# Performance work log

Measured on AMD Instinct MI355X. Metric: run time of the kernel, lower is better.

Reference implementation:

```python
import jax, jax.numpy as jnp
import numpy as np

N, E = 50000, 800000
IN_CH, HID, OUT = 128, 64, 64
H1, H2 = 4, 1
NEG_SLOPE = 0.2  # PyG GATConv default


def _glorot(key, shape):
    fan_in, fan_out = shape[0], shape[-1]
    lim = (6.0 / (fan_in + fan_out)) ** 0.5
    return jax.random.uniform(key, shape, jnp.float32, -lim, lim)


def setup_inputs() -> dict:
    key = jax.random.key(0)
    ks = jax.random.split(key, 12)
    x = jax.random.normal(ks[0], (N, IN_CH), jnp.float32)
    edge_index = jax.random.randint(ks[1], (2, E), 0, N, jnp.int64)
    # layer 1: in_ch -> hid, 4 heads, concat
    W1 = _glorot(ks[2], (IN_CH, H1 * HID))
    a_src1 = _glorot(ks[3], (H1, HID))
    a_dst1 = _glorot(ks[4], (H1, HID))
    b1 = jnp.zeros((H1 * HID,), jnp.float32)
    # layer 2: hid*4 -> out, 1 head, mean (concat=False)
    W2 = _glorot(ks[5], (H1 * HID, H2 * OUT))
    a_src2 = _glorot(ks[6], (H2, OUT))
    a_dst2 = _glorot(ks[7], (H2, OUT))
    b2 = jnp.zeros((OUT,), jnp.float32)
    return {"x": x, "edge_index": edge_index, "W1": W1, "a_src1": a_src1,
            "a_dst1": a_dst1, "b1": b1, "W2": W2, "a_src2": a_src2,
            "a_dst2": a_dst2, "b2": b2}


def gat_layer(x, src, dst, W, a_src, a_dst, b, concat):
    n = x.shape[0]
    Hh, Fh = a_src.shape
    h = (x @ W).reshape(n, Hh, Fh)                      # [N,H,F]
    al_src = jnp.sum(h * a_src[None], axis=-1)          # [N,H]
    al_dst = jnp.sum(h * a_dst[None], axis=-1)          # [N,H]
    logits = jax.nn.leaky_relu(al_src[src] + al_dst[dst], NEG_SLOPE)  # [E,H]
    # numerically stable segment softmax over destination nodes
    mx = jax.ops.segment_max(logits, dst, num_segments=n)
    mx = jnp.where(jnp.isfinite(mx), mx, 0.0)
    e = jnp.exp(logits - mx[dst])                       # [E,H]
    denom = jax.ops.segment_sum(e, dst, num_segments=n)  # [N,H]
    alpha = e / jnp.maximum(denom[dst], 1e-16)          # [E,H]
    msg = h[src] * alpha[:, :, None]                    # [E,H,F]
    out = jax.ops.segment_sum(msg, dst, num_segments=n)  # [N,H,F]
    out = out.reshape(n, Hh * Fh) if concat else out.mean(axis=1)
    return out + b


def reference(x, edge_index, W1, a_src1, a_dst1, b1, W2, a_src2, a_dst2, b2):
    n = x.shape[0]
    # PyG GATConv adds self-loops by default
    loops = jnp.arange(n, dtype=edge_index.dtype)
    src = jnp.concatenate([edge_index[0], loops])
    dst = jnp.concatenate([edge_index[1], loops])
    h = gat_layer(x, src, dst, W1, a_src1, a_dst1, b1, concat=True)
    h = jax.nn.elu(h)
    # dropout is identity in eval mode
    out = gat_layer(h, src, dst, W2, a_src2, a_dst2, b2, concat=False)
    return out
```

## Files before the change

kernel.cpp:

```cpp
#include <hip/hip_runtime.h>
#include <math.h>

#define NEG_SLOPE 0.2f
#define SLOTS 64
#define PARTB 256

typedef unsigned short ushort_t;
typedef _Float16 f16x8 __attribute__((ext_vector_type(8)));
typedef _Float16 h2v  __attribute__((ext_vector_type(2)));
typedef float f32x4v __attribute__((ext_vector_type(4)));

__device__ __forceinline__ float leaky(float x) { return x > 0.f ? x : NEG_SLOPE * x; }

__device__ __forceinline__ ushort_t f2h(float f) {
    union { _Float16 h; ushort_t u; } v; v.h = (_Float16)f; return v.u;
}
__device__ __forceinline__ unsigned packh(float a, float b) {
    union { h2v h; unsigned u; } c; c.h[0] = (_Float16)a; c.h[1] = (_Float16)b; return c.u;
}

__global__ __launch_bounds__(256) void k_prep0A(const float* __restrict__ W1, const float* __restrict__ W2,
                                                const float* __restrict__ as1, const float* __restrict__ ad1,
                                                const float* __restrict__ as2, const float* __restrict__ ad2,
                                                ushort_t* __restrict__ W1t, ushort_t* __restrict__ W2t,
                                                float* __restrict__ va1s, float* __restrict__ va1d,
                                                float* __restrict__ va2s, float* __restrict__ va2d,
                                                const int* __restrict__ ei, int E, int CH, int NBKT,
                                                int* __restrict__ bcnt) {
    __shared__ int hist[256];
    int b = blockIdx.x, t = threadIdx.x;
    if (b >= 322) {
        int k = b - 322;
        hist[t] = 0;
        __syncthreads();
        int i0 = k * CH;
        for (int it = 0; it < CH; it += 256) {
            int i = i0 + it + t;
            if (it + t < CH && i < E) atomicAdd(&hist[ei[E + i] >> 8], 1);
        }
        __syncthreads();
        if (t < NBKT) bcnt[t * PARTB + k] = hist[t];
        return;
    }
    if (b < 256) {
        if (t < 128) W1t[b * 128 + t] = f2h(W1[t * 256 + b]);
    } else if (b < 320) {
        int n = b - 256;
        W2t[n * 256 + t] = f2h(W2[t * 64 + n]);
    } else if (b == 320) {
        for (int idx = t; idx < 1024; idx += 256) {
            int k = idx >> 3, h = (idx >> 1) & 3, sd = idx & 1;
            const float* a = sd ? ad1 : as1;
            float acc = 0.f;
            for (int f = 0; f < 64; ++f) acc += W1[k * 256 + h * 64 + f] * a[h * 64 + f];
            (sd ? va1d : va1s)[k * 4 + h] = acc;
        }
    } else {
        for (int idx = t; idx < 512; idx += 256) {
            int k = idx >> 1, sd = idx & 1;
            const float* a = sd ? ad2 : as2;
            float acc = 0.f;
            for (int f = 0; f < 64; ++f) acc += W2[k * 64 + f] * a[f];
            (sd ? va2d : va2s)[k] = acc;
        }
    }
}

__global__ __launch_bounds__(256) void k_partB1(const int* __restrict__ bcnt,
                                                int* __restrict__ offs, int* __restrict__ btot) {
    __shared__ int wsum[4];
    int t = threadIdx.x, b = blockIdx.x;
    int c = bcnt[b * PARTB + t];
    int lane = t & 63, w = t >> 6;
    int v = c;
    #pragma unroll
    for (int off = 1; off < 64; off <<= 1) {
        int u = __shfl_up(v, off, 64);
        if (lane >= off) v += u;
    }
    if (lane == 63) wsum[w] = v;
    __syncthreads();
    int add = 0;
    for (int ww = 0; ww < w; ++ww) add += wsum[ww];
    offs[b * PARTB + t] = v - c + add;
    if (t == 255) btot[b] = v + add;
}

__global__ __launch_bounds__(256) void k_partB2(const int* __restrict__ btot,
                                                int* __restrict__ bstart, int NBKT, int E) {
    __shared__ int wsum[4];
    int t = threadIdx.x;
    int c = (t < NBKT) ? btot[t] : 0;
    int lane = t & 63, w = t >> 6;
    int v = c;
    #pragma unroll
    for (int off = 1; off < 64; off <<= 1) {
        int u = __shfl_up(v, off, 64);
        if (lane >= off) v += u;
    }
    if (lane == 63) wsum[w] = v;
    __syncthreads();
    int add = 0;
    for (int ww = 0; ww < w; ++ww) add += wsum[ww];
    if (t < NBKT) bstart[t] = v - c + add;
    if (t == 0) bstart[NBKT] = E;
}

__global__ __launch_bounds__(256) void k_partCx(const int* __restrict__ ei, int E, int CH, int NBKT,
                                                const int* __restrict__ offs, const int* __restrict__ bstart,
                                                unsigned* __restrict__ epk,
                                                const float* __restrict__ x,
                                                const float* __restrict__ va1s, const float* __restrict__ va1d,
                                                ushort_t* __restrict__ xh,
                                                float4* __restrict__ alS, float4* __restrict__ alD, int N) {
    __shared__ int cur[256];
    int b = blockIdx.x, t = threadIdx.x;
    if (b < PARTB) {
        int k = b;
        if (t < NBKT) cur[t] = bstart[t] + offs[t * PARTB + k];
        __syncthreads();
        int i0 = k * CH;
        for (int it = 0; it < CH; it += 256) {
            int i = i0 + it + t;
            if (it + t < CH && i < E) {
                unsigned s = (unsigned)ei[i];
                unsigned d = (unsigned)ei[E + i];
                int pos = atomicAdd(&cur[d >> 8], 1);
                epk[pos] = (d << 16) | s;
            }
        }
        return;
    }
    int bb = b - PARTB;
    int r = bb * 16 + (t >> 4);
    int idx = t & 15;
    if (r >= N) return;
    const float* xr = x + (size_t)r * 128 + idx * 8;
    float4 f0 = *(const float4*)xr;
    float4 f1 = *(const float4*)(xr + 4);
    uint4 pv;
    pv.x = packh(f0.x, f0.y); pv.y = packh(f0.z, f0.w);
    pv.z = packh(f1.x, f1.y); pv.w = packh(f1.z, f1.w);
    *(uint4*)&xh[(size_t)r * 128 + idx * 8] = pv;
    float xs[8] = {f0.x, f0.y, f0.z, f0.w, f1.x, f1.y, f1.z, f1.w};
    float s0 = 0, s1 = 0, s2 = 0, s3 = 0, d0 = 0, d1 = 0, d2 = 0, d3 = 0;
    #pragma unroll
    for (int j = 0; j < 8; ++j) {
        int k = idx * 8 + j;
        float4 vs = *(const float4*)&va1s[k * 4];
        float4 vd = *(const float4*)&va1d[k * 4];
        s0 += xs[j] * vs.x; s1 += xs[j] * vs.y; s2 += xs[j] * vs.z; s3 += xs[j] * vs.w;
        d0 += xs[j] * vd.x; d1 += xs[j] * vd.y; d2 += xs[j] * vd.z; d3 += xs[j] * vd.w;
    }
    #pragma unroll
    for (int off = 8; off >= 1; off >>= 1) {
        s0 += __shfl_xor(s0, off, 64); s1 += __shfl_xor(s1, off, 64);
        s2 += __shfl_xor(s2, off, 64); s3 += __shfl_xor(s3, off, 64);
        d0 += __shfl_xor(d0, off, 64); d1 += __shfl_xor(d1, off, 64);
        d2 += __shfl_xor(d2, off, 64); d3 += __shfl_xor(d3, off, 64);
    }
    if (idx == 0) {
        alS[r] = make_float4(s0, s1, s2, s3);
        alD[r] = make_float4(d0, d1, d2, d3);
    }
}

__global__ __launch_bounds__(256) void k_partD(const unsigned* __restrict__ epk, const int* __restrict__ bstart,
                                               int* __restrict__ cnt, ushort_t* __restrict__ csr, int N) {
    __shared__ ushort_t rows[256 * SLOTS];
    __shared__ int cl[256];
    int b = blockIdx.x, t = threadIdx.x;
    for (int i = t; i < 256 * SLOTS / 8; i += 256)
        *(uint4*)&rows[(size_t)i * 8] = make_uint4(0, 0, 0, 0);
    cl[t] = 0;
    __syncthreads();
    int n0 = b * 256;
    if (n0 + t < N) rows[t * SLOTS] = (ushort_t)(n0 + t);
    int e0 = bstart[b], e1 = bstart[b + 1];
    for (int i = e0 + t; i < e1; i += 256) {
        unsigned u = epk[i];
        int dl = (u >> 16) & 255;
        int slot = atomicAdd(&cl[dl], 1);
        if (slot < SLOTS - 1) rows[dl * SLOTS + 1 + slot] = (ushort_t)(u & 0xFFFFu);
    }
    __syncthreads();
    int nvalid = N - n0; if (nvalid > 256) nvalid = 256;
    size_t gbase = (size_t)n0 * SLOTS;
    for (int i = t; i < nvalid * SLOTS / 8; i += 256)
        *(uint4*)(csr + gbase + (size_t)i * 8) = *(const uint4*)&rows[(size_t)i * 8];
    if (t < nvalid) {
        int c = cl[t]; if (c > SLOTS - 1) c = SLOTS - 1;
        cnt[n0 + t] = c;
    }
}

#define CONS(p, a) do { \
    _Float16 ah_ = (_Float16)(a); \
    h2v a2_ = {ah_, ah_}; \
    union { uint4 u; h2v h[4]; } c_; c_.u = (p); \
    ha0 += c_.h[0] * a2_; ha1 += c_.h[1] * a2_; \
    ha2 += c_.h[2] * a2_; ha3 += c_.h[3] * a2_; } while (0)

#define FLUSH() do { \
    acc[0] += (float)ha0[0]; acc[1] += (float)ha0[1]; \
    acc[2] += (float)ha1[0]; acc[3] += (float)ha1[1]; \
    acc[4] += (float)ha2[0]; acc[5] += (float)ha2[1]; \
    acc[6] += (float)ha3[0]; acc[7] += (float)ha3[1]; \
    ha0 = (h2v)0; ha1 = (h2v)0; ha2 = (h2v)0; ha3 = (h2v)0; } while (0)

__global__ __launch_bounds__(256) void k_agg1(const int* __restrict__ cnt, const ushort_t* __restrict__ csr,
                                              const float4* __restrict__ alS4, const float4* __restrict__ alD4,
                                              const ushort_t* __restrict__ xh,
                                              ushort_t* __restrict__ aggh, int N) {
    __shared__ float s_alpha[4][SLOTS][4];
    __shared__ int   s_off[4][SLOTS];
    int w = threadIdx.x >> 6, lane = threadIdx.x & 63;
    int n = blockIdx.x * 4 + w;
    if (n >= N) return;
    int stored = cnt[n]; if (stored > SLOTS - 1) stored = SLOTS - 1;
    int deg = stored + 1;
    int s = 0;
    if (lane < deg) s = csr[(size_t)n * SLOTS + lane];
    s_off[w][lane] = (lane < deg) ? (s << 8) : 0;

    float e0 = 0.f, e1 = 0.f, e2 = 0.f, e3 = 0.f;
    if (lane < deg) {
        float4 ald = alD4[n];
        float4 as = alS4[s];
        e0 = __expf(leaky(as.x + ald.x));
        e1 = __expf(leaky(as.y + ald.y));
        e2 = __expf(leaky(as.z + ald.z));
        e3 = __expf(leaky(as.w + ald.w));
    }
    *(float4*)&s_alpha[w][lane][0] = make_float4(e0, e1, e2, e3);

    int head = lane >> 4, cid = lane & 15;
    const char* xb = (const char*)xh + cid * 16;

    float acc[8];
    #pragma unroll
    for (int i = 0; i < 8; ++i) acc[i] = 0.f;
    h2v ha0 = (h2v)0, ha1 = (h2v)0, ha2 = (h2v)0, ha3 = (h2v)0;

    int nit = (deg + 3) & ~3;

    int4 ovA = *(const int4*)&s_off[w][0];
    uint4 pA0 = *(const uint4*)(xb + ovA.x);
    uint4 pA1 = *(const uint4*)(xb + ovA.y);
    uint4 pA2 = *(const uint4*)(xb + ovA.z);
    uint4 pA3 = *(const uint4*)(xb + ovA.w);

    for (int j = 0; j < nit; j += 8) {
        uint4 pB0, pB1, pB2, pB3;
        bool hasB = (j + 4 < nit);
        if (hasB) {
            int4 ovB = *(const int4*)&s_off[w][j + 4];
            pB0 = *(const uint4*)(xb + ovB.x);
            pB1 = *(const uint4*)(xb + ovB.y);
            pB2 = *(const uint4*)(xb + ovB.z);
            pB3 = *(const uint4*)(xb + ovB.w);
        }
        {
            float a0 = s_alpha[w][j + 0][head];
            float a1 = s_alpha[w][j + 1][head];
            float a2 = s_alpha[w][j + 2][head];
            float a3 = s_alpha[w][j + 3][head];
            CONS(pA0, a0); CONS(pA1, a1); CONS(pA2, a2); CONS(pA3, a3);
        }
        if (hasB) {
            if (j + 8 < nit) {
                int4 ovA2 = *(const int4*)&s_off[w][j + 8];
                pA0 = *(const uint4*)(xb + ovA2.x);
                pA1 = *(const uint4*)(xb + ovA2.y);
                pA2 = *(const uint4*)(xb + ovA2.z);
                pA3 = *(const uint4*)(xb + ovA2.w);
            }
            float a0 = s_alpha[w][j + 4][head];
            float a1 = s_alpha[w][j + 5][head];
            float a2 = s_alpha[w][j + 6][head];
            float a3 = s_alpha[w][j + 7][head];
            CONS(pB0, a0); CONS(pB1, a1); CONS(pB2, a2); CONS(pB3, a3);
        }
        FLUSH();
    }

    float d0 = e0, d1 = e1, d2 = e2, d3 = e3;
    #pragma unroll
    for (int off = 32; off >= 1; off >>= 1) {
        d0 += __shfl_xor(d0, off, 64); d1 += __shfl_xor(d1, off, 64);
        d2 += __shfl_xor(d2, off, 64); d3 += __shfl_xor(d3, off, 64);
    }
    float dh = head == 0 ? d0 : head == 1 ? d1 : head == 2 ? d2 : d3;
    float inv = 1.f / fmaxf(dh, 1e-16f);

    uint4 u;
    u.x = packh(acc[0] * inv, acc[1] * inv);
    u.y = packh(acc[2] * inv, acc[3] * inv);
    u.z = packh(acc[4] * inv, acc[5] * inv);
    u.w = packh(acc[6] * inv, acc[7] * inv);
    *(uint4*)(aggh + (size_t)n * 512 + head * 128 + cid * 8) = u;
}
#undef CONS
#undef FLUSH

__global__ __launch_bounds__(256) void k_g1(const ushort_t* __restrict__ aggh, const ushort_t* __restrict__ W1t,
                                            const float* __restrict__ b1,
                                            const float* __restrict__ va2s, const float* __restrict__ va2d,
                                            ushort_t* __restrict__ out1h,
                                            float* __restrict__ al2S, float* __restrict__ al2D, int N) {
    __shared__ ushort_t sU[4 * 32 * 136];
    __shared__ float s_al2w[4][32][2];
    int t = threadIdx.x;
    int w = t >> 6, lane = t & 63;
    int m = lane & 15, quad = lane >> 4;
    int r0 = blockIdx.x * 32;

    #pragma unroll
    for (int q = 0; q < 8; ++q) {
        int idx = t + q * 256;
        int row = idx >> 6, off = idx & 63;
        int gr = r0 + row;
        uint4 v = (gr < N) ? *(const uint4*)(aggh + (size_t)gr * 512 + off * 8)
                           : make_uint4(0, 0, 0, 0);
        int h = off >> 4, k8 = off & 15;
        *(uint4*)&sU[(size_t)(h * 32 + row) * 136 + k8 * 8] = v;
    }
    __syncthreads();

    f32x4v acc[2][4];
    #pragma unroll
    for (int r = 0; r < 2; ++r)
        #pragma unroll
        for (int cg = 0; cg < 4; ++cg) acc[r][cg] = (f32x4v){0.f, 0.f, 0.f, 0.f};
    #pragma unroll
    for (int ks = 0; ks < 4; ++ks) {
        f16x8 af[2];
        #pragma unroll
        for (int r = 0; r < 2; ++r)
            af[r] = *(f16x8*)&sU[(size_t)(w * 32 + r * 16 + m) * 136 + ks * 32 + quad * 8];
        #pragma unroll
        for (int cg = 0; cg < 4; ++cg) {
            f16x8 bf = *(f16x8*)&W1t[(size_t)(w * 64 + cg * 16 + m) * 128 + ks * 32 + quad * 8];
            #pragma unroll
            for (int r = 0; r < 2; ++r)
                acc[r][cg] = __builtin_amdgcn_mfma_f32_16x16x32_f16(af[r], bf, acc[r][cg], 0, 0, 0);
        }
    }

    float ps[2][4], pd[2][4];
    #pragma unroll
    for (int r = 0; r < 2; ++r)
        #pragma unroll
        for (int reg = 0; reg < 4; ++reg) { ps[r][reg] = 0.f; pd[r][reg] = 0.f; }
    #pragma unroll
    for (int cg = 0; cg < 4; ++cg) {
        int c = w * 64 + cg * 16 + m;
        float bias = b1[c];
        float v2s = va2s[c], v2d = va2d[c];
        #pragma unroll
        for (int r = 0; r < 2; ++r)
            #pragma unroll
            for (int reg = 0; reg < 4; ++reg) {
                int row = r * 16 + quad * 4 + reg;
                int gr = r0 + row;
                float v = acc[r][cg][reg] + bias;
                v = v > 0.f ? v : (__expf(v) - 1.f);
                if (gr < N) out1h[(size_t)gr * 256 + c] = f2h(v);
                ps[r][reg] += v * v2s;
                pd[r][reg] += v * v2d;
            }
    }
    #pragma unroll
    for (int off = 1; off <= 8; off <<= 1)
        #pragma unroll
        for (int r = 0; r < 2; ++r)
            #pragma unroll
            for (int reg = 0; reg < 4; ++reg) {
                ps[r][reg] += __shfl_xor(ps[r][reg], off, 64);
                pd[r][reg] += __shfl_xor(pd[r][reg], off, 64);
            }
    if (m == 0) {
        #pragma unroll
        for (int r = 0; r < 2; ++r)
            #pragma unroll
            for (int reg = 0; reg < 4; ++reg) {
                int row = r * 16 + quad * 4 + reg;
                s_al2w[w][row][0] = ps[r][reg];
                s_al2w[w][row][1] = pd[r][reg];
            }
    }
    __syncthreads();
    if (t < 32) {
        int gr = r0 + t;
        if (gr < N) {
            float a = 0.f, b = 0.f;
            #pragma unroll
            for (int w2 = 0; w2 < 4; ++w2) { a += s_al2w[w2][t][0]; b += s_al2w[w2][t][1]; }
            al2S[gr] = a; al2D[gr] = b;
        }
    }
}

__global__ __launch_bounds__(256) void k_g2(const ushort_t* __restrict__ in, const ushort_t* __restrict__ W2t,
                                            ushort_t* __restrict__ h2h, int N) {
    __shared__ ushort_t As[64 * 136];
    __shared__ ushort_t Bs[64 * 136];
    int t = threadIdx.x;
    int r0 = blockIdx.x * 64;
    int w = t >> 6, lane = t & 63;
    int m = lane & 15, quad = lane >> 4;
    f32x4v acc[4];
    #pragma unroll
    for (int r = 0; r < 4; ++r) acc[r] = (f32x4v){0.f, 0.f, 0.f, 0.f};
    for (int kb = 0; kb < 2; ++kb) {
        #pragma unroll
        for (int q = 0; q < 4; ++q) {
            int idx = t + q * 256;
            int row = idx >> 4, off = idx & 15;
            int gr = r0 + row;
            uint4 v = (gr < N) ? *(const uint4*)(in + (size_t)gr * 256 + kb * 128 + off * 8)
                               : make_uint4(0, 0, 0, 0);
            *(uint4*)&As[row * 136 + off * 8] = v;
        }
        #pragma unroll
        for (int q = 0; q < 4; ++q) {
            int idx = t + q * 256;
            int row = idx >> 4, off = idx & 15;
            uint4 v = *(const uint4*)(W2t + (size_t)row * 256 + kb * 128 + off * 8);
            *(uint4*)&Bs[row * 136 + off * 8] = v;
        }
        __syncthreads();
        #pragma unroll
        for (int ks = 0; ks < 4; ++ks) {
            int k0 = ks * 32 + quad * 8;
            f16x8 af[4], bfr;
            #pragma unroll
            for (int r = 0; r < 4; ++r) af[r] = *(f16x8*)&As[(r * 16 + m) * 136 + k0];
            bfr = *(f16x8*)&Bs[(w * 16 + m) * 136 + k0];
            #pragma unroll
            for (int r = 0; r < 4; ++r)
                acc[r] = __builtin_amdgcn_mfma_f32_16x16x32_f16(af[r], bfr, acc[r], 0, 0, 0);
        }
        __syncthreads();
    }
    int col = w * 16 + m;
    #pragma unroll
    for (int r = 0; r < 4; ++r) {
        int gr0 = r0 + r * 16 + quad * 4;
        #pragma unroll
        for (int reg = 0; reg < 4; ++reg) {
            int gr = gr0 + reg;
            if (gr < N) h2h[(size_t)gr * 64 + col] = f2h(acc[r][reg]);
        }
    }
}

__global__ __launch_bounds__(256) void k_agg2(const int* __restrict__ cnt, const ushort_t* __restrict__ csr,
                                              const float* __restrict__ alS, const float* __restrict__ alD,
                                              const ushort_t* __restrict__ h2h, const float* __restrict__ b2,
                                              float* __restrict__ out, int N) {
    int lane = threadIdx.x & 63;
    int n = blockIdx.x * 4 + (threadIdx.x >> 6);
    if (n >= N) return;
    int stored = cnt[n]; if (stored > SLOTS - 1) stored = SLOTS - 1;
    int deg = stored + 1;
    const ushort_t* crow = csr + (size_t)n * SLOTS;

    int s0 = 0;
    if (lane < deg) s0 = crow[lane];

    int grp = lane >> 3, cid = lane & 7;
    int choff = cid * 16;
    const char* hbase = (const char*)h2h;

    uint4 pbuf[3];
    #pragma unroll
    for (int i = 0; i < 3; ++i) {
        int sj = __shfl(s0, i * 8 + grp, 64);
        pbuf[i] = *(const uint4*)(hbase + ((size_t)sj << 7) + choff);
    }

    float ald = alD[n];
    float e0 = 0.f;
    if (lane < deg) e0 = __expf(leaky(alS[s0] + ald));

    h2v ha0 = (h2v)0, ha1 = (h2v)0, ha2 = (h2v)0, ha3 = (h2v)0;
    #pragma unroll
    for (int i = 0; i < 3; ++i) {
        float a = __shfl(e0, i * 8 + grp, 64);
        union { uint4 u; h2v h[4]; } c; c.u = pbuf[i];
        _Float16 ah = (_Float16)a;
        h2v a2 = {ah, ah};
        ha0 += c.h[0] * a2; ha1 += c.h[1] * a2;
        ha2 += c.h[2] * a2; ha3 += c.h[3] * a2;
    }
    for (int j = 24; j < deg; j += 8) {
        int jj = j + grp;
        float a = __shfl(e0, jj, 64);
        int sj = __shfl(s0, jj, 64);
        union { uint4 u; h2v h[4]; } c;
        c.u = *(const uint4*)(hbase + ((size_t)sj << 7) + choff);
        _Float16 ah = (_Float16)a;
        h2v a2 = {ah, ah};
        ha0 += c.h[0] * a2; ha1 += c.h[1] * a2;
        ha2 += c.h[2] * a2; ha3 += c.h[3] * a2;
    }

    float den = e0;
    #pragma unroll
    for (int off = 32; off >= 1; off >>= 1) den += __shfl_xor(den, off, 64);
    float inv = 1.f / fmaxf(den, 1e-16f);

    float acc[8];
    acc[0] = (float)ha0[0]; acc[1] = (float)ha0[1];
    acc[2] = (float)ha1[0]; acc[3] = (float)ha1[1];
    acc[4] = (float)ha2[0]; acc[5] = (float)ha2[1];
    acc[6] = (float)ha3[0]; acc[7] = (float)ha3[1];
    #pragma unroll
    for (int off = 8; off <= 32; off <<= 1)
        #pragma unroll
        for (int i = 0; i < 8; ++i) acc[i] += __shfl_xor(acc[i], off, 64);

    if (grp == 0) {
        int c8 = cid * 8;
        float4 b0 = *(const float4*)&b2[c8];
        float4 b1v = *(const float4*)&b2[c8 + 4];
        float4 o0 = make_float4(acc[0]*inv + b0.x, acc[1]*inv + b0.y, acc[2]*inv + b0.z, acc[3]*inv + b0.w);
        float4 o1 = make_float4(acc[4]*inv + b1v.x, acc[5]*inv + b1v.y, acc[6]*inv + b1v.z, acc[7]*inv + b1v.w);
        *(float4*)(out + (size_t)n * 64 + c8) = o0;
        *(float4*)(out + (size_t)n * 64 + c8 + 4) = o1;
    }
}

extern "C" void kernel_launch(void* const* d_in, const int* in_sizes, int n_in,
                              void* d_out, int out_size, void* d_ws, size_t ws_size,
                              hipStream_t stream) {
    const float* x      = (const float*)d_in[0];
    const int*   ei     = (const int*)d_in[1];
    const float* W1     = (const float*)d_in[2];
    const float* a_src1 = (const float*)d_in[3];
    const float* a_dst1 = (const float*)d_in[4];
    const float* b1     = (const float*)d_in[5];
    const float* W2     = (const float*)d_in[6];
    const float* a_src2 = (const float*)d_in[7];
    const float* a_dst2 = (const float*)d_in[8];
    const float* b2     = (const float*)d_in[9];
    float* out = (float*)d_out;

    int N = in_sizes[0] / 128;
    int E = in_sizes[1] / 2;

    char* ws = (char*)d_ws;
    size_t off = 0;
    auto alloc = [&](size_t bytes) -> void* {
        void* p = ws + off;
        off = (off + bytes + 255) & ~(size_t)255;
        return p;
    };
    ushort_t* xh    = (ushort_t*)alloc((size_t)N * 128 * 2);
    ushort_t* aggh  = (ushort_t*)alloc((size_t)N * 512 * 2);
    ushort_t* out1h = (ushort_t*)alloc((size_t)N * 256 * 2);
    ushort_t* h2h   = (ushort_t*)alloc((size_t)N * 64 * 2);
    ushort_t* W1t   = (ushort_t*)alloc(256 * 128 * 2);
    ushort_t* W2t   = (ushort_t*)alloc(64 * 256 * 2);
    float* va1s  = (float*)alloc(128 * 4 * 4);
    float* va1d  = (float*)alloc(128 * 4 * 4);
    float* va2s  = (float*)alloc(256 * 4);
    float* va2d  = (float*)alloc(256 * 4);
    float* alS1  = (float*)alloc((size_t)N * 4 * 4);
    float* alD1  = (float*)alloc((size_t)N * 4 * 4);
    float* alS2  = (float*)alloc((size_t)N * 4);
    float* alD2  = (float*)alloc((size_t)N * 4);
    int*   cnt   = (int*)alloc((size_t)N * 4);
    ushort_t* csr = (ushort_t*)alloc((size_t)N * SLOTS * 2);
    int NBKT = (N + 255) >> 8;
    int*      bcnt  = (int*)alloc((size_t)NBKT * PARTB * 4);
    int*      offs  = (int*)alloc((size_t)NBKT * PARTB * 4);
    int*      btot  = (int*)alloc((size_t)NBKT * 4);
    int*      bstart= (int*)alloc((size_t)(NBKT + 1) * 4);
    unsigned* epk   = (unsigned*)alloc((size_t)E * 4);
    (void)ws_size; (void)n_in; (void)out_size;

    int CH  = (E + PARTB - 1) / PARTB;
    int XB  = (N + 15) / 16;
    int AB1 = (N + 3) / 4;
    int G1  = (N + 31) / 32;
    int G2  = (N + 63) / 64;
    int NC4 = (N + 3) / 4;

    k_prep0A<<<322 + PARTB, 256, 0, stream>>>(W1, W2, a_src1, a_dst1, a_src2, a_dst2,
                                              W1t, W2t, va1s, va1d, va2s, va2d,
                                              ei, E, CH, NBKT, bcnt);
    k_partB1<<<NBKT, 256, 0, stream>>>(bcnt, offs, btot);
    k_partB2<<<1, 256, 0, stream>>>(btot, bstart, NBKT, E);
    k_partCx<<<PARTB + XB, 256, 0, stream>>>(ei, E, CH, NBKT, offs, bstart, epk,
                                             x, va1s, va1d, xh, (float4*)alS1, (float4*)alD1, N);
    k_partD<<<NBKT, 256, 0, stream>>>(epk, bstart, cnt, csr, N);
    k_agg1<<<AB1, 256, 0, stream>>>(cnt, csr,
                                    (const float4*)alS1, (const float4*)alD1,
                                    xh, aggh, N);
    k_g1<<<G1, 256, 0, stream>>>(aggh, W1t, b1, va2s, va2d, out1h, alS2, alD2, N);
    k_g2<<<G2, 256, 0, stream>>>(out1h, W2t, h2h, N);
    k_agg2<<<NC4, 256, 0, stream>>>(cnt, csr, alS2, alD2, h2h, b2, out, N);
}
```

Before: 238.6 us.

## Fuse graph-build prep kernels into one persistent kernel with grid barriers

Merges the five preprocessing kernels (histogram/transpose, two scans, scatter plus x conversion, CSR build) into one 256-block kernel that uses atomic-counter grid barriers between phases. This removes four kernel launch gaps and drains, and overlaps the x fp16 conversion and attention-logit work with the scan phases. In exchange it relies on all 256 blocks being co-resident for the spin barriers, adds a memset, and reads x twice in separate passes.

```diff
diff --git a/kernel.cpp b/kernel.cpp
--- a/kernel.cpp
+++ b/kernel.cpp
@@ -19,35 +19,55 @@
     union { h2v h; unsigned u; } c; c.h[0] = (_Float16)a; c.h[1] = (_Float16)b; return c.u;
 }
 
-__global__ __launch_bounds__(256) void k_prep0A(const float* __restrict__ W1, const float* __restrict__ W2,
-                                                const float* __restrict__ as1, const float* __restrict__ ad1,
-                                                const float* __restrict__ as2, const float* __restrict__ ad2,
-                                                ushort_t* __restrict__ W1t, ushort_t* __restrict__ W2t,
-                                                float* __restrict__ va1s, float* __restrict__ va1d,
-                                                float* __restrict__ va2s, float* __restrict__ va2d,
-                                                const int* __restrict__ ei, int E, int CH, int NBKT,
-                                                int* __restrict__ bcnt) {
+__device__ __forceinline__ void gbar(int* g, int id) {
+    __syncthreads();
+    if (threadIdx.x == 0) {
+        __threadfence();
+        if (atomicAdd(&g[id * 2], 1) == PARTB - 1) {
+            atomicExch(&g[id * 2 + 1], 1);
+        } else {
+            while (atomicAdd(&g[id * 2 + 1], 0) == 0) __builtin_amdgcn_s_sleep(1);
+        }
+        __threadfence();
+    }
+    __syncthreads();
+}
+
+__global__ __launch_bounds__(256) void k_build(const float* __restrict__ W1, const float* __restrict__ W2,
+                                               const float* __restrict__ as1, const float* __restrict__ ad1,
+                                               const float* __restrict__ as2, const float* __restrict__ ad2,
+                                               ushort_t* __restrict__ W1t, ushort_t* __restrict__ W2t,
+                                               float* __restrict__ va1s, float* __restrict__ va1d,
+                                               float* __restrict__ va2s, float* __restrict__ va2d,
+                                               const int* __restrict__ ei, int E, int CH, int NBKT,
+                                               int* __restrict__ bcnt, int* __restrict__ offs,
+                                               int* __restrict__ btot, int* __restrict__ bstart,
+                                               unsigned* __restrict__ epk,
+                                               const float* __restrict__ x, ushort_t* __restrict__ xh,
+                                               float4* __restrict__ alS, float4* __restrict__ alD,
+                                               int* __restrict__ cnt, ushort_t* __restrict__ csr,
+                                               int N, int* __restrict__ gsync) {
+    __shared__ ushort_t rows[256 * SLOTS];
+    __shared__ int cl[256];
     __shared__ int hist[256];
+    __shared__ int cur[256];
+    __shared__ int wsum[4];
     int b = blockIdx.x, t = threadIdx.x;
-    if (b >= 322) {
-        int k = b - 322;
-        hist[t] = 0;
-        __syncthreads();
-        int i0 = k * CH;
+
+    hist[t] = 0;
+    __syncthreads();
+    {
+        int i0 = b * CH;
         for (int it = 0; it < CH; it += 256) {
             int i = i0 + it + t;
             if (it + t < CH && i < E) atomicAdd(&hist[ei[E + i] >> 8], 1);
         }
-        __syncthreads();
-        if (t < NBKT) bcnt[t * PARTB + k] = hist[t];
-        return;
-    }
-    if (b < 256) {
-        if (t < 128) W1t[b * 128 + t] = f2h(W1[t * 256 + b]);
-    } else if (b < 320) {
-        int n = b - 256;
-        W2t[n * 256 + t] = f2h(W2[t * 64 + n]);
-    } else if (b == 320) {
+    }
+    __syncthreads();
+    if (t < NBKT) bcnt[t * PARTB + b] = hist[t];
+    if (t < 128) W1t[b * 128 + t] = f2h(W1[t * 256 + b]);
+    if (b < 64)  W2t[b * 256 + t] = f2h(W2[t * 64 + b]);
+    if (b == 64) {
         for (int idx = t; idx < 1024; idx += 256) {
             int k = idx >> 3, h = (idx >> 1) & 3, sd = idx & 1;
             const float* a = sd ? ad1 : as1;
@@ -55,7 +75,8 @@
             for (int f = 0; f < 64; ++f) acc += W1[k * 256 + h * 64 + f] * a[h * 64 + f];
             (sd ? va1d : va1s)[k * 4 + h] = acc;
         }
-    } else {
+    }
+    if (b == 65) {
         for (int idx = t; idx < 512; idx += 256) {
             int k = idx >> 1, sd = idx & 1;
             const float* a = sd ? ad2 : as2;
@@ -64,62 +85,91 @@
             (sd ? va2d : va2s)[k] = acc;
         }
     }
-}
-
-__global__ __launch_bounds__(256) void k_partB1(const int* __restrict__ bcnt,
-                                                int* __restrict__ offs, int* __restrict__ btot) {
-    __shared__ int wsum[4];
-    int t = threadIdx.x, b = blockIdx.x;
-    int c = bcnt[b * PARTB + t];
-    int lane = t & 63, w = t >> 6;
-    int v = c;
-    #pragma unroll
-    for (int off = 1; off < 64; off <<= 1) {
-        int u = __shfl_up(v, off, 64);
-        if (lane >= off) v += u;
-    }
-    if (lane == 63) wsum[w] = v;
+    for (int pass = 0; pass < 13; ++pass) {
+        int r = (pass * 256 + b) * 16 + (t >> 4);
+        int idx = t & 15;
+        if (r < N) {
+            const float* xr = x + (size_t)r * 128 + idx * 8;
+            float4 f0 = *(const float4*)xr;
+            float4 f1 = *(const float4*)(xr + 4);
+            uint4 pv;
+            pv.x = packh(f0.x, f0.y); pv.y = packh(f0.z, f0.w);
+            pv.z = packh(f1.x, f1.y); pv.w = packh(f1.z, f1.w);
+            *(uint4*)&xh[(size_t)r * 128 + idx * 8] = pv;
+        }
+    }
+    gbar(gsync, 0);
+
+    if (b < NBKT) {
+        int c = bcnt[b * PARTB + t];
+        int lane = t & 63, w = t >> 6;
+        int v = c;
+        #pragma unroll
+        for (int off = 1; off < 64; off <<= 1) {
+            int u = __shfl_up(v, off, 64);
+            if (lane >= off) v += u;
+        }
+        if (lane == 63) wsum[w] = v;
+        __syncthreads();
+        int add = 0;
+        for (int ww = 0; ww < w; ++ww) add += wsum[ww];
+        offs[b * PARTB + t] = v - c + add;
+        if (t == 255) btot[b] = v + add;
+    }
+    for (int pass = 0; pass < 13; ++pass) {
+        int r = (pass * 256 + b) * 16 + (t >> 4);
+        int idx = t & 15;
+        if (r < N) {
+            const float* xr = x + (size_t)r * 128 + idx * 8;
+            float4 f0 = *(const float4*)xr;
+            float4 f1 = *(const float4*)(xr + 4);
+            float xs[8] = {f0.x, f0.y, f0.z, f0.w, f1.x, f1.y, f1.z, f1.w};
+            float s0 = 0, s1 = 0, s2 = 0, s3 = 0, d0 = 0, d1 = 0, d2 = 0, d3 = 0;
+            #pragma unroll
+            for (int j = 0; j < 8; ++j) {
+                int k = idx * 8 + j;
+                float4 vs = *(const float4*)&va1s[k * 4];
+                float4 vd = *(const float4*)&va1d[k * 4];
+                s0 += xs[j] * vs.x; s1 += xs[j] * vs.y; s2 += xs[j] * vs.z; s3 += xs[j] * vs.w;
+                d0 += xs[j] * vd.x; d1 += xs[j] * vd.y; d2 += xs[j] * vd.z; d3 += xs[j] * vd.w;
+            }
+            #pragma unroll
+            for (int off = 8; off >= 1; off >>= 1) {
+                s0 += __shfl_xor(s0, off, 64); s1 += __shfl_xor(s1, off, 64);
+                s2 += __shfl_xor(s2, off, 64); s3 += __shfl_xor(s3, off, 64);
+                d0 += __shfl_xor(d0, off, 64); d1 += __shfl_xor(d1, off, 64);
+                d2 += __shfl_xor(d2, off, 64); d3 += __shfl_xor(d3, off, 64);
+            }
+            if (idx == 0) {
+                alS[r] = make_float4(s0, s1, s2, s3);
+                alD[r] = make_float4(d0, d1, d2, d3);
+            }
+        }
+    }
+    gbar(gsync, 1);
+
+    if (b == 0) {
+        int c = (t < NBKT) ? btot[t] : 0;
+        int lane = t & 63, w = t >> 6;
+        int v = c;
+        #pragma unroll
+        for (int off = 1; off < 64; off <<= 1) {
+            int u = __shfl_up(v, off, 64);
+            if (lane >= off) v += u;
+        }
+        if (lane == 63) wsum[w] = v;
+        __syncthreads();
+        int add = 0;
+        for (int ww = 0; ww < w; ++ww) add += wsum[ww];
+        if (t < NBKT) bstart[t] = v - c + add;
+        if (t == 0) bstart[NBKT] = E;
+    }
+    gbar(gsync, 2);
+
+    if (t < NBKT) cur[t] = bstart[t] + offs[t * PARTB + b];
     __syncthreads();
-    int add = 0;
-    for (int ww = 0; ww < w; ++ww) add += wsum[ww];
-    offs[b * PARTB + t] = v - c + add;
-    if (t == 255) btot[b] = v + add;
-}
-
-__global__ __launch_bounds__(256) void k_partB2(const int* __restrict__ btot,
-                                                int* __restrict__ bstart, int NBKT, int E) {
-    __shared__ int wsum[4];
-    int t = threadIdx.x;
-    int c = (t < NBKT) ? btot[t] : 0;
-    int lane = t & 63, w = t >> 6;
-    int v = c;
-    #pragma unroll
-    for (int off = 1; off < 64; off <<= 1) {
-        int u = __shfl_up(v, off, 64);
-        if (lane >= off) v += u;
-    }
-    if (lane == 63) wsum[w] = v;
-    __syncthreads();
-    int add = 0;
-    for (int ww = 0; ww < w; ++ww) add += wsum[ww];
-    if (t < NBKT) bstart[t] = v - c + add;
-    if (t == 0) bstart[NBKT] = E;
-}
-
-__global__ __launch_bounds__(256) void k_partCx(const int* __restrict__ ei, int E, int CH, int NBKT,
-                                                const int* __restrict__ offs, const int* __restrict__ bstart,
-                                                unsigned* __restrict__ epk,
-                                                const float* __restrict__ x,
-                                                const float* __restrict__ va1s, const float* __restrict__ va1d,
-                                                ushort_t* __restrict__ xh,
-                                                float4* __restrict__ alS, float4* __restrict__ alD, int N) {
-    __shared__ int cur[256];
-    int b = blockIdx.x, t = threadIdx.x;
-    if (b < PARTB) {
-        int k = b;
-        if (t < NBKT) cur[t] = bstart[t] + offs[t * PARTB + k];
-        __syncthreads();
-        int i0 = k * CH;
+    {
+        int i0 = b * CH;
         for (int it = 0; it < CH; it += 256) {
             int i = i0 + it + t;
             if (it + t < CH && i < E) {
@@ -129,68 +179,32 @@
                 epk[pos] = (d << 16) | s;
             }
         }
-        return;
-    }
-    int bb = b - PARTB;
-    int r = bb * 16 + (t >> 4);
-    int idx = t & 15;
-    if (r >= N) return;
-    const float* xr = x + (size_t)r * 128 + idx * 8;
-    float4 f0 = *(const float4*)xr;
-    float4 f1 = *(const float4*)(xr + 4);
-    uint4 pv;
-    pv.x = packh(f0.x, f0.y); pv.y = packh(f0.z, f0.w);
-    pv.z = packh(f1.x, f1.y); pv.w = packh(f1.z, f1.w);
-    *(uint4*)&xh[(size_t)r * 128 + idx * 8] = pv;
-    float xs[8] = {f0.x, f0.y, f0.z, f0.w, f1.x, f1.y, f1.z, f1.w};
-    float s0 = 0, s1 = 0, s2 = 0, s3 = 0, d0 = 0, d1 = 0, d2 = 0, d3 = 0;
-    #pragma unroll
-    for (int j = 0; j < 8; ++j) {
-        int k = idx * 8 + j;
-        float4 vs = *(const float4*)&va1s[k * 4];
-        float4 vd = *(const float4*)&va1d[k * 4];
-        s0 += xs[j] * vs.x; s1 += xs[j] * vs.y; s2 += xs[j] * vs.z; s3 += xs[j] * vs.w;
-        d0 += xs[j] * vd.x; d1 += xs[j] * vd.y; d2 += xs[j] * vd.z; d3 += xs[j] * vd.w;
-    }
-    #pragma unroll
-    for (int off = 8; off >= 1; off >>= 1) {
-        s0 += __shfl_xor(s0, off, 64); s1 += __shfl_xor(s1, off, 64);
-        s2 += __shfl_xor(s2, off, 64); s3 += __shfl_xor(s3, off, 64);
-        d0 += __shfl_xor(d0, off, 64); d1 += __shfl_xor(d1, off, 64);
-        d2 += __shfl_xor(d2, off, 64); d3 += __shfl_xor(d3, off, 64);
-    }
-    if (idx == 0) {
-        alS[r] = make_float4(s0, s1, s2, s3);
-        alD[r] = make_float4(d0, d1, d2, d3);
-    }
-}
-
-__global__ __launch_bounds__(256) void k_partD(const unsigned* __restrict__ epk, const int* __restrict__ bstart,
-                                               int* __restrict__ cnt, ushort_t* __restrict__ csr, int N) {
-    __shared__ ushort_t rows[256 * SLOTS];
-    __shared__ int cl[256];
-    int b = blockIdx.x, t = threadIdx.x;
-    for (int i = t; i < 256 * SLOTS / 8; i += 256)
-        *(uint4*)&rows[(size_t)i * 8] = make_uint4(0, 0, 0, 0);
-    cl[t] = 0;
-    __syncthreads();
-    int n0 = b * 256;
-    if (n0 + t < N) rows[t * SLOTS] = (ushort_t)(n0 + t);
-    int e0 = bstart[b], e1 = bstart[b + 1];
-    for (int i = e0 + t; i < e1; i += 256) {
-        unsigned u = epk[i];
-        int dl = (u >> 16) & 255;
-        int slot = atomicAdd(&cl[dl], 1);
-        if (slot < SLOTS - 1) rows[dl * SLOTS + 1 + slot] = (ushort_t)(u & 0xFFFFu);
-    }
-    __syncthreads();
-    int nvalid = N - n0; if (nvalid > 256) nvalid = 256;
-    size_t gbase = (size_t)n0 * SLOTS;
-    for (int i = t; i < nvalid * SLOTS / 8; i += 256)
-        *(uint4*)(csr + gbase + (size_t)i * 8) = *(const uint4*)&rows[(size_t)i * 8];
-    if (t < nvalid) {
-        int c = cl[t]; if (c > SLOTS - 1) c = SLOTS - 1;
-        cnt[n0 + t] = c;
+    }
+    gbar(gsync, 3);
+
+    if (b < NBKT) {
+        for (int i = t; i < 256 * SLOTS / 8; i += 256)
+            *(uint4*)&rows[(size_t)i * 8] = make_uint4(0, 0, 0, 0);
+        cl[t] = 0;
+        __syncthreads();
+        int n0 = b * 256;
+        if (n0 + t < N) rows[t * SLOTS] = (ushort_t)(n0 + t);
+        int e0 = bstart[b], e1 = bstart[b + 1];
+        for (int i = e0 + t; i < e1; i += 256) {
+            unsigned u = epk[i];
+            int dl = (u >> 16) & 255;
+            int slot = atomicAdd(&cl[dl], 1);
+            if (slot < SLOTS - 1) rows[dl * SLOTS + 1 + slot] = (ushort_t)(u & 0xFFFFu);
+        }
+        __syncthreads();
+        int nvalid = N - n0; if (nvalid > 256) nvalid = 256;
+        size_t gbase = (size_t)n0 * SLOTS;
+        for (int i = t; i < nvalid * SLOTS / 8; i += 256)
+            *(uint4*)(csr + gbase + (size_t)i * 8) = *(const uint4*)&rows[(size_t)i * 8];
+        if (t < nvalid) {
+            int c = cl[t]; if (c > SLOTS - 1) c = SLOTS - 1;
+            cnt[n0 + t] = c;
+        }
     }
 }
 
@@ -579,23 +593,20 @@
     int*      btot  = (int*)alloc((size_t)NBKT * 4);
     int*      bstart= (int*)alloc((size_t)(NBKT + 1) * 4);
     unsigned* epk   = (unsigned*)alloc((size_t)E * 4);
+    int*      gsync = (int*)alloc(64);
     (void)ws_size; (void)n_in; (void)out_size;
 
     int CH  = (E + PARTB - 1) / PARTB;
-    int XB  = (N + 15) / 16;
     int AB1 = (N + 3) / 4;
     int G1  = (N + 31) / 32;
     int G2  = (N + 63) / 64;
     int NC4 = (N + 3) / 4;
 
-    k_prep0A<<<322 + PARTB, 256, 0, stream>>>(W1, W2, a_src1, a_dst1, a_src2, a_dst2,
-                                              W1t, W2t, va1s, va1d, va2s, va2d,
-                                              ei, E, CH, NBKT, bcnt);
-    k_partB1<<<NBKT, 256, 0, stream>>>(bcnt, offs, btot);
-    k_partB2<<<1, 256, 0, stream>>>(btot, bstart, NBKT, E);
-    k_partCx<<<PARTB + XB, 256, 0, stream>>>(ei, E, CH, NBKT, offs, bstart, epk,
-                                             x, va1s, va1d, xh, (float4*)alS1, (float4*)alD1, N);
-    k_partD<<<NBKT, 256, 0, stream>>>(epk, bstart, cnt, csr, N);
+    hipMemsetAsync(gsync, 0, 64, stream);
+    k_build<<<PARTB, 256, 0, stream>>>(W1, W2, a_src1, a_dst1, a_src2, a_dst2,
+                                       W1t, W2t, va1s, va1d, va2s, va2d,
+                                       ei, E, CH, NBKT, bcnt, offs, btot, bstart, epk,
+                                       x, xh, (float4*)alS1, (float4*)alD1, cnt, csr, N, gsync);
     k_agg1<<<AB1, 256, 0, stream>>>(cnt, csr,
                                     (const float4*)alS1, (const float4*)alD1,
                                     xh, aggh, N);
```

New measurement: 327.6 us. 1.37x slower.
